# Kernel optimization log

Hardware: AMD Instinct MI355X
Metric: run time of the kernel (lower is better)

## Reference

```python
import jax, jax.numpy as jnp
import numpy as np

N_NODES = 100000
N_FEAT = 512
HIDDEN = 16
N_CLASSES = 7
N_EDGES = 3200000


def gcn_conv(x, W, b, src, dst, num_nodes):
    """GCNConv: add self-loops, symmetric deg^-1/2 normalization, linear, aggregate."""
    loop = jnp.arange(num_nodes, dtype=src.dtype)
    src2 = jnp.concatenate([src, loop])  # [E+N]
    dst2 = jnp.concatenate([dst, loop])
    ones = jnp.ones(src2.shape[0], dtype=x.dtype)
    deg = jax.ops.segment_sum(ones, dst2, num_segments=num_nodes)  # in-degree incl. self-loop
    dinv = jnp.where(deg > 0, jax.lax.rsqrt(deg), 0.0)
    norm = dinv[src2] * dinv[dst2]  # [E+N]
    h = x @ W  # [N, out] -- transform before gather (small out dim)
    msg = h[src2] * norm[:, None]  # gather + scale
    out = jax.ops.segment_sum(msg, dst2, num_segments=num_nodes)  # scatter-add
    return out + b


def setup_inputs() -> dict:
    key = jax.random.key(0)
    k1, k2, k3, k4, k5 = jax.random.split(key, 5)
    x = jax.random.normal(k1, (N_NODES, N_FEAT), dtype=jnp.float32)
    edge_index = jax.random.randint(k2, (2, N_EDGES), 0, N_NODES, dtype=jnp.int64)
    # Glorot init like PyG GCNConv
    W1 = jax.random.normal(k3, (N_FEAT, HIDDEN), dtype=jnp.float32) * np.sqrt(2.0 / (N_FEAT + HIDDEN))
    b1 = jnp.zeros((HIDDEN,), dtype=jnp.float32)
    W2 = jax.random.normal(k4, (HIDDEN, N_CLASSES), dtype=jnp.float32) * np.sqrt(2.0 / (HIDDEN + N_CLASSES))
    b2 = jnp.zeros((N_CLASSES,), dtype=jnp.float32)
    return {"x": x, "edge_index": edge_index, "W1": W1, "b1": b1, "W2": W2, "b2": b2}


def reference(x, edge_index, W1, b1, W2, b2):
    src, dst = edge_index[0], edge_index[1]
    h = gcn_conv(x, W1, b1, src, dst, N_NODES)
    h = jax.nn.relu(h)
    # F.dropout(training=self.training): identity in eval mode (deterministic reference)
    h = gcn_conv(h, W2, b2, src, dst, N_NODES)
    return jax.nn.log_softmax(h, axis=1)
```

## Files before the change

### kernel.cpp

```cpp
#include <hip/hip_runtime.h>
#include <math.h>

#define N_NODES   100000
#define N_FEAT    512
#define HIDDEN    16
#define N_CLASSES 7
#define N_EDGES   3200000

#define BSHIFT 7
#define BNODES 128
#define BMASK  127
#define NBUK   782
#define CHUNK  16384
#define NCHUNK 196
#define CAP    6144

typedef short v8s __attribute__((ext_vector_type(8)));
typedef float v4f __attribute__((ext_vector_type(4)));

__device__ __forceinline__ float bf_lo(unsigned int p) { return __uint_as_float(p << 16); }
__device__ __forceinline__ float bf_hi(unsigned int p) { return __uint_as_float(p & 0xffff0000u); }
__device__ __forceinline__ unsigned int pack_bf2(float a, float b) {
    unsigned int ua = __float_as_uint(a); ua += 0x7fffu + ((ua >> 16) & 1u);
    unsigned int ub = __float_as_uint(b); ub += 0x7fffu + ((ub >> 16) & 1u);
    return (ua >> 16) | (ub & 0xffff0000u);
}


__global__ __launch_bounds__(256) void k_wpack(const float* __restrict__ W1,
                                               unsigned int* __restrict__ wfrag_g) {
    int tid = threadIdx.x;
    int q0 = tid * 4;
#pragma unroll
    for (int qq = 0; qq < 4; qq++) {
        int q = q0 + qq;
        int s = q >> 6, l = q & 63;
        int n = l & 15, kb = s * 32 + (l >> 4) * 8;
        unsigned int* wp = &wfrag_g[q * 4];
#pragma unroll
        for (int h = 0; h < 4; h++)
            wp[h] = pack_bf2(W1[(kb + 2 * h) * 16 + n],
                             W1[(kb + 2 * h + 1) * 16 + n]);
    }
}


__global__ __launch_bounds__(1024) void k_hist(const int* __restrict__ dst,
                                               int* __restrict__ hglob) {
    __shared__ int h[NBUK];
    int tid = threadIdx.x;
    for (int i = tid; i < NBUK; i += 1024) h[i] = 0;
    __syncthreads();
    int base = blockIdx.x * CHUNK;
    for (int i = tid; i < CHUNK; i += 1024) {
        int e = base + i;
        if (e < N_EDGES) atomicAdd(&h[dst[e] >> BSHIFT], 1);
    }
    __syncthreads();
    for (int i = tid; i < NBUK; i += 1024)
        hglob[blockIdx.x * NBUK + i] = h[i];
}


__global__ __launch_bounds__(1024) void k_scan(const int* __restrict__ hglob,
                                               int* __restrict__ btot,
                                               int* __restrict__ gbase,
                                               int* __restrict__ hpre) {
    __shared__ int sd[1024];
    int t = threadIdx.x;
    int tot = 0;
    if (t < NBUK)
        for (int c = 0; c < NCHUNK; c++) tot += hglob[c * NBUK + t];
    sd[t] = (t < NBUK) ? tot : 0;
    __syncthreads();
    for (int off = 1; off < 1024; off <<= 1) {
        int a = (t >= off) ? sd[t - off] : 0;
        __syncthreads();
        sd[t] += a;
        __syncthreads();
    }
    if (t < NBUK) {
        int ex = sd[t] - tot;
        btot[t] = tot;
        gbase[t] = ex;
        int run = ex;
        for (int c = 0; c < NCHUNK; c++) {
            hpre[c * NBUK + t] = run;
            run += hglob[c * NBUK + t];
        }
    }
}


__global__ __launch_bounds__(1024) void k_scatter(const int* __restrict__ src,
                                                  const int* __restrict__ dst,
                                                  const int* __restrict__ hpre,
                                                  int* __restrict__ entries) {
    __shared__ int lb[NBUK];
    __shared__ int cur[NBUK];
    __shared__ int lbase[NBUK];
    __shared__ int sd[1024];
    __shared__ int sbuf[CHUNK];
    __shared__ unsigned short sbk[CHUNK];
    int tid = threadIdx.x;
    int base = blockIdx.x * CHUNK;

    for (int i = tid; i < NBUK; i += 1024) {
        lb[i] = hpre[blockIdx.x * NBUK + i];
        cur[i] = 0;
    }
    __syncthreads();

    int myent[16];
    int mypos[16];
#pragma unroll
    for (int u = 0; u < 16; u++) {
        int e = base + u * 1024 + tid;
        int en = 0, bp = -1;
        if (e < N_EDGES) {
            int d = dst[e];
            int b = d >> BSHIFT;
            int r = atomicAdd(&cur[b], 1);
            en = src[e] | ((d & BMASK) << 17);
            bp = (b << 14) | r;
        }
        myent[u] = en;
        mypos[u] = bp;
    }
    __syncthreads();

    int v = (tid < NBUK) ? cur[tid] : 0;
    sd[tid] = v;
    __syncthreads();
    for (int off = 1; off < 1024; off <<= 1) {
        int a = (tid >= off) ? sd[tid - off] : 0;
        __syncthreads();
        sd[tid] += a;
        __syncthreads();
    }
    if (tid < NBUK) lbase[tid] = sd[tid] - v;
    __syncthreads();

#pragma unroll
    for (int u = 0; u < 16; u++) {
        int bp = mypos[u];
        if (bp >= 0) {
            int b = bp >> 14, r = bp & 0x3FFF;
            int p = lbase[b] + r;
            sbuf[p] = myent[u];
            sbk[p] = (unsigned short)b;
        }
    }
    __syncthreads();

    int lim = N_EDGES - base;
    if (lim > CHUNK) lim = CHUNK;
    for (int i = tid; i < lim; i += 1024) {
        int b = sbk[i];
        entries[lb[b] + (i - lbase[b])] = sbuf[i];
    }
}


__global__ __launch_bounds__(256) void k_deg(const int* __restrict__ entries,
                                             const int* __restrict__ btot,
                                             const int* __restrict__ gbase,
                                             float* __restrict__ dinv) {
    __shared__ int hcnt[BNODES];
    int tid = threadIdx.x;
    int bk = blockIdx.x;
    if (tid < BNODES) hcnt[tid] = 0;
    __syncthreads();
    int cnt = btot[bk], base = gbase[bk];
    for (int i = tid; i < cnt; i += 256)
        atomicAdd(&hcnt[entries[base + i] >> 17], 1);
    __syncthreads();
    if (tid < BNODES) {
        int n = bk * BNODES + tid;
        if (n < N_NODES) dinv[n] = rsqrtf((float)(hcnt[tid] + 1));
    }
}


__global__ __launch_bounds__(256) void k_gemm1(const float* __restrict__ x,
                                               const unsigned int* __restrict__ wfrag_g,
                                               const float* __restrict__ dinv,
                                               unsigned int* __restrict__ hs1b) {
    __shared__ unsigned int wfrag[16 * 64 * 4];
    __shared__ float dtile[4 * 16 * 17];

    int tid = threadIdx.x;
    int wave = tid >> 6, lane = tid & 63;
    int row0 = blockIdx.x * 64;
    int m = lane & 15, quad = lane >> 4;

    {
        const uint4* wg = (const uint4*)wfrag_g;
        uint4* wl = (uint4*)wfrag;
        for (int i = tid; i < 1024; i += 256) wl[i] = wg[i];
    }

    int grow = row0 + wave * 16 + m;
    bool vrow = (grow < N_NODES);
    const float* xr = x + (size_t)(vrow ? grow : 0) * N_FEAT + quad * 8;

    v4f acc = {0.f, 0.f, 0.f, 0.f};
    __syncthreads();

#pragma unroll
    for (int c = 0; c < 16; c++) {
        float4 xa = make_float4(0.f, 0.f, 0.f, 0.f);
        float4 xb = make_float4(0.f, 0.f, 0.f, 0.f);
        if (vrow) {
            xa = *(const float4*)(xr + c * 32);
            xb = *(const float4*)(xr + c * 32 + 4);
        }
        unsigned int pa[4] = {pack_bf2(xa.x, xa.y), pack_bf2(xa.z, xa.w),
                              pack_bf2(xb.x, xb.y), pack_bf2(xb.z, xb.w)};
        v8s af;
        __builtin_memcpy(&af, pa, 16);
        v8s bf = *(const v8s*)&wfrag[(c * 64 + lane) * 4];
        acc = __builtin_amdgcn_mfma_f32_16x16x32_bf16(af, bf, acc, 0, 0, 0);
    }

    {
        float* wdt = dtile + wave * 272;
#pragma unroll
        for (int r = 0; r < 4; r++)
            wdt[(quad * 4 + r) * 17 + m] = acc[r];
    }
    __syncthreads();
    {
        int row = tid >> 2, p = tid & 3;
        int orow = row0 + row;
        if (orow < N_NODES) {
            float dn = dinv[orow];
            float* wdt = dtile + (row >> 4) * 272 + (row & 15) * 17 + 4 * p;
            unsigned int d0 = pack_bf2(dn * wdt[0], dn * wdt[1]);
            unsigned int d1 = pack_bf2(dn * wdt[2], dn * wdt[3]);
            *(uint2*)(hs1b + (size_t)orow * 8 + 2 * p) = make_uint2(d0, d1);
        }
    }
}


__global__ __launch_bounds__(512) void k_agg1(const unsigned int* __restrict__ hs1b,
                                              int* __restrict__ entries,
                                              const int* __restrict__ btot,
                                              const int* __restrict__ gbase,
                                              const float* __restrict__ dinv,
                                              const float* __restrict__ b1,
                                              const float* __restrict__ W2,
                                              unsigned int* __restrict__ hs2b,
                                              int* __restrict__ nodeptr) {
    __shared__ int ebuf[CAP];
    __shared__ int hcnt[BNODES];
    __shared__ int hincl[BNODES];
    __shared__ int hcur[BNODES];
    __shared__ float w2l[HIDDEN * N_CLASSES];
    __shared__ float b1l[HIDDEN];
    __shared__ float part[BNODES][17];
    int tid = threadIdx.x;
    int bk = blockIdx.x;
    if (tid < HIDDEN * N_CLASSES) w2l[tid] = W2[tid];
    if (tid < HIDDEN) b1l[tid] = b1[tid];
    if (tid < BNODES) hcnt[tid] = 0;
    int cnt = btot[bk], base = gbase[bk];
    if (cnt > CAP) cnt = CAP;
    __syncthreads();

    for (int i = tid; i < cnt; i += 512) {
        int en = entries[base + i];
        ebuf[i] = en;
        atomicAdd(&hcnt[en >> 17], 1);
    }
    __syncthreads();
    if (tid < BNODES) hincl[tid] = hcnt[tid];
    __syncthreads();
    for (int off = 1; off < BNODES; off <<= 1) {
        int v = 0;
        if (tid < BNODES && tid >= off) v = hincl[tid - off];
        __syncthreads();
        if (tid < BNODES) hincl[tid] += v;
        __syncthreads();
    }
    if (tid < BNODES) {
        int excl = hincl[tid] - hcnt[tid];
        hcur[tid] = excl;
        int n = bk * BNODES + tid;
        if (n <= N_NODES) nodeptr[n] = base + excl;
    }
    __syncthreads();
    for (int i = tid; i < cnt; i += 512) {
        int en = ebuf[i];
        int pos = atomicAdd(&hcur[en >> 17], 1);
        entries[base + pos] = en & 0x1FFFF;
    }
    __syncthreads();

    int g = tid >> 1, j = tid & 1;
    int l = g & (BNODES - 1), half = g >> 7;
    int n = bk * BNODES + l;
    bool valid = (n < N_NODES);

    float accL[4] = {0.f, 0.f, 0.f, 0.f};
    float accH[4] = {0.f, 0.f, 0.f, 0.f};
    const uint4* hv = (const uint4*)hs1b;
    const int* srt = entries;

    if (valid) {
        int p0 = base + hincl[l] - hcnt[l];
        int p1 = base + hincl[l];
        int mid = p0 + ((p1 - p0) >> 1);
        int e0 = half ? mid : p0;
        int e1 = half ? p1 : mid;
        int e = e0;
        for (; e + 4 <= e1; e += 4) {
            int s[4];
            uint4 v[4];
#pragma unroll
            for (int u = 0; u < 4; u++) s[u] = srt[e + u];
#pragma unroll
            for (int u = 0; u < 4; u++) v[u] = hv[(size_t)s[u] * 2 + j];
#pragma unroll
            for (int u = 0; u < 4; u++) {
                accL[0] += bf_lo(v[u].x); accH[0] += bf_hi(v[u].x);
                accL[1] += bf_lo(v[u].y); accH[1] += bf_hi(v[u].y);
                accL[2] += bf_lo(v[u].z); accH[2] += bf_hi(v[u].z);
                accL[3] += bf_lo(v[u].w); accH[3] += bf_hi(v[u].w);
            }
        }
        for (; e < e1; e++) {
            uint4 v0 = hv[(size_t)srt[e] * 2 + j];
            accL[0] += bf_lo(v0.x); accH[0] += bf_hi(v0.x);
            accL[1] += bf_lo(v0.y); accH[1] += bf_hi(v0.y);
            accL[2] += bf_lo(v0.z); accH[2] += bf_hi(v0.z);
            accL[3] += bf_lo(v0.w); accH[3] += bf_hi(v0.w);
        }
        if (half == 0) {
            uint4 sv = hv[(size_t)n * 2 + j];
            accL[0] += bf_lo(sv.x); accH[0] += bf_hi(sv.x);
            accL[1] += bf_lo(sv.y); accH[1] += bf_hi(sv.y);
            accL[2] += bf_lo(sv.z); accH[2] += bf_hi(sv.z);
            accL[3] += bf_lo(sv.w); accH[3] += bf_hi(sv.w);
        }
    }

    if (half == 1 && valid) {
#pragma unroll
        for (int q = 0; q < 4; q++) {
            int ch = j * 8 + 2 * q;
            part[l][ch]     = accL[q];
            part[l][ch + 1] = accH[q];
        }
    }
    __syncthreads();

    if (half == 0 && valid) {
        float dn = dinv[n];
        float t[7] = {0.f, 0.f, 0.f, 0.f, 0.f, 0.f, 0.f};
#pragma unroll
        for (int q = 0; q < 4; q++) {
            int ch = j * 8 + 2 * q;
            float z0 = fmaxf(dn * (accL[q] + part[l][ch])     + b1l[ch],     0.f);
            float z1 = fmaxf(dn * (accH[q] + part[l][ch + 1]) + b1l[ch + 1], 0.f);
            const float* w0 = &w2l[ch * 7];
            const float* w1 = &w2l[(ch + 1) * 7];
#pragma unroll
            for (int k = 0; k < 7; k++) t[k] += z0 * w0[k] + z1 * w1[k];
        }
#pragma unroll
        for (int k = 0; k < 7; k++) t[k] += __shfl_xor(t[k], 1, 64);
        if (j == 0) {
            uint4 o;
            o.x = pack_bf2(dn * t[0], dn * t[1]);
            o.y = pack_bf2(dn * t[2], dn * t[3]);
            o.z = pack_bf2(dn * t[4], dn * t[5]);
            o.w = pack_bf2(dn * t[6], 0.f);
            ((uint4*)hs2b)[n] = o;
        }
    }
}


__global__ __launch_bounds__(512) void k_agg2(const unsigned int* __restrict__ hs2b,
                                              const int* __restrict__ srt,
                                              const int* __restrict__ nodeptr,
                                              const float* __restrict__ dinv,
                                              const float* __restrict__ b2,
                                              float* __restrict__ out) {
    int tid = threadIdx.x;
    int bk = blockIdx.x;
    int l = tid >> 2, h = tid & 3;
    int n = bk * BNODES + l;
    bool valid = (n < N_NODES);

    float a[8] = {0.f, 0.f, 0.f, 0.f, 0.f, 0.f, 0.f, 0.f};
    const uint4* hv = (const uint4*)hs2b;

    if (valid) {
        int p0 = nodeptr[n], p1 = nodeptr[n + 1];
        int deg = p1 - p0;
        int e0 = p0 + ((deg * h) >> 2);
        int e1 = p0 + ((deg * (h + 1)) >> 2);
        int e = e0;
        for (; e + 4 <= e1; e += 4) {
            int s[4];
            uint4 v[4];
#pragma unroll
            for (int u = 0; u < 4; u++) s[u] = srt[e + u];
#pragma unroll
            for (int u = 0; u < 4; u++) v[u] = hv[s[u]];
#pragma unroll
            for (int u = 0; u < 4; u++) {
                a[0] += bf_lo(v[u].x); a[1] += bf_hi(v[u].x);
                a[2] += bf_lo(v[u].y); a[3] += bf_hi(v[u].y);
                a[4] += bf_lo(v[u].z); a[5] += bf_hi(v[u].z);
                a[6] += bf_lo(v[u].w);
            }
        }
        for (; e < e1; e++) {
            uint4 v0 = hv[srt[e]];
            a[0] += bf_lo(v0.x); a[1] += bf_hi(v0.x);
            a[2] += bf_lo(v0.y); a[3] += bf_hi(v0.y);
            a[4] += bf_lo(v0.z); a[5] += bf_hi(v0.z);
            a[6] += bf_lo(v0.w);
        }
        if (h == 0) {
            uint4 sv = hv[n];
            a[0] += bf_lo(sv.x); a[1] += bf_hi(sv.x);
            a[2] += bf_lo(sv.y); a[3] += bf_hi(sv.y);
            a[4] += bf_lo(sv.z); a[5] += bf_hi(sv.z);
            a[6] += bf_lo(sv.w);
        }
#pragma unroll
        for (int q = 0; q < 7; q++) {
            a[q] += __shfl_xor(a[q], 1, 64);
            a[q] += __shfl_xor(a[q], 2, 64);
        }
        if (h == 0) {
            float dn = dinv[n];
            float lg[7];
#pragma unroll
            for (int c = 0; c < 7; c++) lg[c] = dn * a[c] + b2[c];
            float m = lg[0];
#pragma unroll
            for (int c = 1; c < 7; c++) m = fmaxf(m, lg[c]);
            float s = 0.f;
#pragma unroll
            for (int c = 0; c < 7; c++) s += expf(lg[c] - m);
            float ls = m + logf(s);
#pragma unroll
            for (int c = 0; c < 7; c++) out[(size_t)n * 7 + c] = lg[c] - ls;
        }
    }
}


extern "C" void kernel_launch(void* const* d_in, const int* in_sizes, int n_in,
                              void* d_out, int out_size, void* d_ws, size_t ws_size,
                              hipStream_t stream) {
    const float* x  = (const float*)d_in[0];
    const int*   ei = (const int*)d_in[1];
    const float* W1 = (const float*)d_in[2];
    const float* b1 = (const float*)d_in[3];
    const float* W2 = (const float*)d_in[4];
    const float* b2 = (const float*)d_in[5];
    float* out = (float*)d_out;

    const int* src = ei;
    const int* dst = ei + N_EDGES;

    char* w = (char*)d_ws;
    int*          btot    = (int*)(w + 0);
    int*          gbase   = (int*)(w + 4096);
    float*        dinv    = (float*)(w + 8192);
    int*          nodeptr = (int*)(w + 408576);
    int*          hglob   = (int*)(w + 808960);
    int*          hpre    = (int*)(w + 1422336);
    unsigned int* hs1b    = (unsigned int*)(w + 2036736);
    unsigned int* hs2b    = (unsigned int*)(w + 5236736);
    int*          entries = (int*)(w + 6836736);
    unsigned int* wfrag_g = (unsigned int*)(w + 19636736);

    k_wpack   <<<1, 256, 0, stream>>>(W1, wfrag_g);
    k_hist    <<<NCHUNK, 1024, 0, stream>>>(dst, hglob);
    k_scan    <<<1, 1024, 0, stream>>>(hglob, btot, gbase, hpre);
    k_scatter <<<NCHUNK, 1024, 0, stream>>>(src, dst, hpre, entries);
    k_deg     <<<NBUK, 256, 0, stream>>>(entries, btot, gbase, dinv);
    k_gemm1   <<<1563, 256, 0, stream>>>(x, wfrag_g, dinv, hs1b);
    k_agg1    <<<NBUK, 512, 0, stream>>>(hs1b, entries, btot, gbase, dinv, b1, W2, hs2b, nodeptr);
    k_agg2    <<<NBUK, 512, 0, stream>>>(hs2b, entries, nodeptr, dinv, b2, out);
}
```

Measured before the change: 442.3 us.

## Parallelize bucket-prefix scan across blocks and fold weight packing into histogram

```diff
diff --git a/kernel.cpp b/kernel.cpp
--- a/kernel.cpp
+++ b/kernel.cpp
@@ -26,29 +26,33 @@
     return (ua >> 16) | (ub & 0xffff0000u);
 }
 
-
-__global__ __launch_bounds__(256) void k_wpack(const float* __restrict__ W1,
+__device__ __forceinline__ int wincl(int v, int lane) {
+#pragma unroll
+    for (int off = 1; off < 64; off <<= 1) {
+        int u = __shfl_up(v, off, 64);
+        if (lane >= off) v += u;
+    }
+    return v;
+}
+
+
+__global__ __launch_bounds__(1024) void k_hist(const int* __restrict__ dst,
+                                               int* __restrict__ hglob,
+                                               const float* __restrict__ W1,
                                                unsigned int* __restrict__ wfrag_g) {
+    __shared__ int h[NBUK];
     int tid = threadIdx.x;
-    int q0 = tid * 4;
-#pragma unroll
-    for (int qq = 0; qq < 4; qq++) {
-        int q = q0 + qq;
+    if (blockIdx.x == NCHUNK) {
+        int q = tid;
         int s = q >> 6, l = q & 63;
         int n = l & 15, kb = s * 32 + (l >> 4) * 8;
         unsigned int* wp = &wfrag_g[q * 4];
 #pragma unroll
-        for (int h = 0; h < 4; h++)
-            wp[h] = pack_bf2(W1[(kb + 2 * h) * 16 + n],
-                             W1[(kb + 2 * h + 1) * 16 + n]);
-    }
-}
-
-
-__global__ __launch_bounds__(1024) void k_hist(const int* __restrict__ dst,
-                                               int* __restrict__ hglob) {
-    __shared__ int h[NBUK];
-    int tid = threadIdx.x;
+        for (int hh = 0; hh < 4; hh++)
+            wp[hh] = pack_bf2(W1[(kb + 2 * hh) * 16 + n],
+                              W1[(kb + 2 * hh + 1) * 16 + n]);
+        return;
+    }
     for (int i = tid; i < NBUK; i += 1024) h[i] = 0;
     __syncthreads();
     int base = blockIdx.x * CHUNK;
@@ -62,51 +66,57 @@
 }
 
 
-__global__ __launch_bounds__(1024) void k_scan(const int* __restrict__ hglob,
-                                               int* __restrict__ btot,
-                                               int* __restrict__ gbase,
-                                               int* __restrict__ hpre) {
-    __shared__ int sd[1024];
+__global__ __launch_bounds__(256) void k_hpre(const int* __restrict__ hglob,
+                                              int* __restrict__ hpre,
+                                              int* __restrict__ btot) {
+    __shared__ int wsum[4];
+    int b = blockIdx.x;
     int t = threadIdx.x;
-    int tot = 0;
-    if (t < NBUK)
-        for (int c = 0; c < NCHUNK; c++) tot += hglob[c * NBUK + t];
-    sd[t] = (t < NBUK) ? tot : 0;
-    __syncthreads();
-    for (int off = 1; off < 1024; off <<= 1) {
-        int a = (t >= off) ? sd[t - off] : 0;
-        __syncthreads();
-        sd[t] += a;
-        __syncthreads();
-    }
-    if (t < NBUK) {
-        int ex = sd[t] - tot;
-        btot[t] = tot;
-        gbase[t] = ex;
-        int run = ex;
-        for (int c = 0; c < NCHUNK; c++) {
-            hpre[c * NBUK + t] = run;
-            run += hglob[c * NBUK + t];
-        }
-    }
+    int lane = t & 63, w = t >> 6;
+    int v = (t < NCHUNK) ? hglob[t * NBUK + b] : 0;
+    int inc = wincl(v, lane);
+    if (lane == 63) wsum[w] = inc;
+    __syncthreads();
+    int off = 0;
+#pragma unroll
+    for (int k = 0; k < 4; k++) off += (k < w) ? wsum[k] : 0;
+    int excl = off + inc - v;
+    if (t < NCHUNK) hpre[t * NBUK + b] = excl;
+    if (t == NCHUNK - 1) btot[b] = excl + v;
+}
+
+
+__global__ __launch_bounds__(1024) void k_scan(const int* __restrict__ btot,
+                                               int* __restrict__ gbase) {
+    __shared__ int wsum[16];
+    int t = threadIdx.x, lane = t & 63, w = t >> 6;
+    int v = (t < NBUK) ? btot[t] : 0;
+    int inc = wincl(v, lane);
+    if (lane == 63) wsum[w] = inc;
+    __syncthreads();
+    int off = 0;
+#pragma unroll
+    for (int k = 0; k < 16; k++) off += (k < w) ? wsum[k] : 0;
+    if (t < NBUK) gbase[t] = off + inc - v;
 }
 
 
 __global__ __launch_bounds__(1024) void k_scatter(const int* __restrict__ src,
                                                   const int* __restrict__ dst,
                                                   const int* __restrict__ hpre,
+                                                  const int* __restrict__ gbase,
                                                   int* __restrict__ entries) {
     __shared__ int lb[NBUK];
     __shared__ int cur[NBUK];
     __shared__ int lbase[NBUK];
-    __shared__ int sd[1024];
+    __shared__ int wsum[16];
     __shared__ int sbuf[CHUNK];
     __shared__ unsigned short sbk[CHUNK];
     int tid = threadIdx.x;
     int base = blockIdx.x * CHUNK;
 
     for (int i = tid; i < NBUK; i += 1024) {
-        lb[i] = hpre[blockIdx.x * NBUK + i];
+        lb[i] = gbase[i] + hpre[blockIdx.x * NBUK + i];
         cur[i] = 0;
     }
     __syncthreads();
@@ -129,17 +139,18 @@
     }
     __syncthreads();
 
-    int v = (tid < NBUK) ? cur[tid] : 0;
-    sd[tid] = v;
-    __syncthreads();
-    for (int off = 1; off < 1024; off <<= 1) {
-        int a = (tid >= off) ? sd[tid - off] : 0;
+    {
+        int lane = tid & 63, w = tid >> 6;
+        int v = (tid < NBUK) ? cur[tid] : 0;
+        int inc = wincl(v, lane);
+        if (lane == 63) wsum[w] = inc;
         __syncthreads();
-        sd[tid] += a;
+        int off = 0;
+#pragma unroll
+        for (int k = 0; k < 16; k++) off += (k < w) ? wsum[k] : 0;
+        if (tid < NBUK) lbase[tid] = off + inc - v;
         __syncthreads();
     }
-    if (tid < NBUK) lbase[tid] = sd[tid] - v;
-    __syncthreads();
 
 #pragma unroll
     for (int u = 0; u < 16; u++) {
@@ -483,10 +494,10 @@
     int*          entries = (int*)(w + 6836736);
     unsigned int* wfrag_g = (unsigned int*)(w + 19636736);
 
-    k_wpack   <<<1, 256, 0, stream>>>(W1, wfrag_g);
-    k_hist    <<<NCHUNK, 1024, 0, stream>>>(dst, hglob);
-    k_scan    <<<1, 1024, 0, stream>>>(hglob, btot, gbase, hpre);
-    k_scatter <<<NCHUNK, 1024, 0, stream>>>(src, dst, hpre, entries);
+    k_hist    <<<NCHUNK + 1, 1024, 0, stream>>>(dst, hglob, W1, wfrag_g);
+    k_hpre    <<<NBUK, 256, 0, stream>>>(hglob, hpre, btot);
+    k_scan    <<<1, 1024, 0, stream>>>(btot, gbase);
+    k_scatter <<<NCHUNK, 1024, 0, stream>>>(src, dst, hpre, gbase, entries);
     k_deg     <<<NBUK, 256, 0, stream>>>(entries, btot, gbase, dinv);
     k_gemm1   <<<1563, 256, 0, stream>>>(x, wfrag_g, dinv, hs1b);
     k_agg1    <<<NBUK, 512, 0, stream>>>(hs1b, entries, btot, gbase, dinv, b1, W2, hs2b, nodeptr);
```

Result: faster. 423.6 us (-4.2%).
